# Optimization experiments

Measured on AMD Instinct MI355X. Metric: run time of the kernel, lower is better.

## Reference

```python
import jax, jax.numpy as jnp
import numpy as np

LEAK = 0.01


def setup_inputs() -> dict:
    key = jax.random.key(0)
    k1, k2, k3, k4 = jax.random.split(key, 4)
    N, I, O, H, E = 20000, 128, 128, 4, 320000
    input_h = jax.random.normal(k1, (N, I), dtype=jnp.float32)
    edges = jax.random.randint(k2, (E, 3), 0, N, dtype=jnp.int64)
    # xavier-normal-ish scale for W (H,O,I) and a (H,1,2O)
    W = jax.random.normal(k3, (H, O, I), dtype=jnp.float32) * np.float32(np.sqrt(2.0 / (O + I)))
    a = jax.random.normal(k4, (H, 1, 2 * O), dtype=jnp.float32) * np.float32(np.sqrt(2.0 / (1 + 2 * O)))
    return {"input_h": input_h, "edges": edges, "W": W, "a": a}


def reference(input_h, edges, W, a):
    H, O, _ = W.shape
    N = input_h.shape[0]
    src, rel, dst = edges[:, 0], edges[:, 1], edges[:, 2]
    # per-head projection: x[h,n,o] = sum_i W[h,o,i] * input_h[n,i]
    x = jnp.einsum('hoi,ni->hno', W, input_h)            # (H,N,O)
    h = x.sum(axis=0) / H                                # (N,O)
    # attention scores: (cat([x_src, x_dst]) * a).sum(-1), split a to avoid the concat
    a_src = a[:, 0, :O]                                  # (H,O)
    a_dst = a[:, 0, O:]                                  # (H,O)
    x_dst = x[:, dst]                                    # (H,E,O)
    scores = jnp.einsum('heo,ho->he', x[:, src], a_src) + jnp.einsum('heo,ho->he', x_dst, a_dst)
    # NOTE: faithful to original — softmax is over ALL edges per head
    att = jax.nn.softmax(jax.nn.leaky_relu(scores, LEAK), axis=-1)  # (H,E)
    message = (x_dst * att[..., None]).reshape(-1, O)    # (H*E, O), head-major like torch.cat
    src_rep = jnp.tile(src, H)                           # (H*E,)
    agg = jax.ops.segment_sum(message, src_rep, num_segments=N)  # (N,O)
    return h + agg / H
```

## Files before the change

### kernel.cpp

```cpp
#include <hip/hip_runtime.h>

#define NF 128
#define NH 4
#define BCAP 64

typedef __attribute__((ext_vector_type(4))) float f32x4;
typedef __attribute__((ext_vector_type(8))) short bf16x8;

#define FP4C 0.7f
#define FP4INV (1.0f / FP4C)

__device__ __forceinline__ float b2f(unsigned short u) {
  return __uint_as_float(((unsigned)u) << 16);
}
__device__ __forceinline__ unsigned short f2b(float f) {
  unsigned u = __float_as_uint(f);
  unsigned r = ((u >> 16) & 1u) + 0x7fffu;
  return (unsigned short)((u + r) >> 16);
}

__global__ __launch_bounds__(256) void k_prep0(
    const float* __restrict__ W, unsigned short* __restrict__ Wfhi) {
  int i = blockIdx.x * 256 + threadIdx.x;
  int h = i >> 11, rem = i & 2047;
  int o = rem >> 4, i0 = (rem & 15) * 8;
  const float* p = W + (size_t)(h * NF + o) * NF + i0;
  float4 a = *(const float4*)p, b = *(const float4*)(p + 4);
  float vv[8] = {a.x, a.y, a.z, a.w, b.x, b.y, b.z, b.w};
  bf16x8 hi8;
  #pragma unroll
  for (int j = 0; j < 8; ++j) hi8[j] = (short)f2b(vv[j]);
  int rec = (((o >> 4) * 4 + h) * 4 + (i0 >> 5)) * 64 +
            ((i0 >> 3) & 3) * 16 + (o & 15);
  *(bf16x8*)(Wfhi + (size_t)rec * 8) = hi8;
}

__global__ __launch_bounds__(256) void k1_mfma(
    const float* __restrict__ inp, const unsigned short* __restrict__ Wfhi,
    const float* __restrict__ ag, unsigned int* __restrict__ x4,
    float* __restrict__ s4s, float* __restrict__ s4d,
    float* __restrict__ out, int* __restrict__ cnt, int N) {
  __shared__ unsigned short sAhi[4 * 64 * 8];
  __shared__ unsigned short sAlo[4 * 64 * 8];
  __shared__ unsigned short xL[32 * 64 * 4];
  const int t = threadIdx.x, w = t >> 6, l = t & 63;
  const int col = l & 15, quad = l >> 4;
  const int n0 = blockIdx.x * 16;

  if (t < 16) cnt[n0 + t] = 0;

  {
    const float* p = inp + (size_t)(n0 + col) * NF + w * 32 + quad * 8;
    float4 v0 = *(const float4*)p, v1 = *(const float4*)(p + 4);
    float vv[8] = {v0.x, v0.y, v0.z, v0.w, v1.x, v1.y, v1.z, v1.w};
    bf16x8 hi8, lo8;
    #pragma unroll
    for (int j = 0; j < 8; ++j) {
      unsigned short hi = f2b(vv[j]);
      hi8[j] = (short)hi;
      lo8[j] = (short)f2b(vv[j] - b2f(hi));
    }
    *(bf16x8*)(sAhi + (w * 64 + l) * 8) = hi8;
    *(bf16x8*)(sAlo + (w * 64 + l) * 8) = lo8;
  }
  __syncthreads();

  bf16x8 Ah[4], Al[4];
  #pragma unroll
  for (int s = 0; s < 4; ++s) {
    Ah[s] = *(bf16x8*)(sAhi + (s * 64 + l) * 8);
    Al[s] = *(bf16x8*)(sAlo + (s * 64 + l) * 8);
  }

  float as8[8], ad8[8];
  #pragma unroll
  for (int ot = 0; ot < 8; ++ot) {
    as8[ot] = ag[w * 2 * NF + ot * 16 + col];
    ad8[ot] = ag[w * 2 * NF + NF + ot * 16 + col];
  }

  const bf16x8* WH = (const bf16x8*)Wfhi;
  bf16x8 cur[4];
  #pragma unroll
  for (int s = 0; s < 4; ++s) cur[s] = WH[(size_t)((0 * 4 + w) * 4 + s) * 64 + l];

  float ps[4] = {0.f, 0.f, 0.f, 0.f}, pd[4] = {0.f, 0.f, 0.f, 0.f};
  #pragma unroll
  for (int ot = 0; ot < 8; ++ot) {
    bf16x8 nxt[4];
    if (ot < 7) {
      #pragma unroll
      for (int s = 0; s < 4; ++s)
        nxt[s] = WH[(size_t)(((ot + 1) * 4 + w) * 4 + s) * 64 + l];
    }
    f32x4 acc = {0.f, 0.f, 0.f, 0.f};
    #pragma unroll
    for (int s = 0; s < 4; ++s) {
      acc = __builtin_amdgcn_mfma_f32_16x16x32_bf16(Al[s], cur[s], acc, 0, 0, 0);
      acc = __builtin_amdgcn_mfma_f32_16x16x32_bf16(Ah[s], cur[s], acc, 0, 0, 0);
    }
    ushort4 xs;
    #pragma unroll
    for (int r = 0; r < 4; ++r) {
      ps[r] = fmaf(acc[r], as8[ot], ps[r]);
      pd[r] = fmaf(acc[r], ad8[ot], pd[r]);
    }
    xs.x = f2b(acc[0]); xs.y = f2b(acc[1]);
    xs.z = f2b(acc[2]); xs.w = f2b(acc[3]);
    *(ushort4*)(xL + ((w * 8 + ot) * 64 + l) * 4) = xs;
    if (ot < 7) {
      #pragma unroll
      for (int s = 0; s < 4; ++s) cur[s] = nxt[s];
    }
  }

  #pragma unroll
  for (int m = 1; m < 16; m <<= 1)
    #pragma unroll
    for (int r = 0; r < 4; ++r) {
      ps[r] += __shfl_xor(ps[r], m);
      pd[r] += __shfl_xor(pd[r], m);
    }
  if (col == 0) {
    #pragma unroll
    for (int r = 0; r < 4; ++r) {
      int n = n0 + quad * 4 + r;
      s4s[n * 4 + w] = ps[r];
      s4d[n * 4 + w] = pd[r];
    }
  }
  __syncthreads();

  {
    int c2 = t & 7, qd = (t >> 3) & 3, ot = t >> 5;
    float xv[4][4][2];
    #pragma unroll
    for (int h = 0; h < NH; ++h) {
      int slab = h * 8 + ot;
      ushort4 qa = *(const ushort4*)(xL + (slab * 64 + qd * 16 + c2 * 2) * 4);
      ushort4 qb = *(const ushort4*)(xL + (slab * 64 + qd * 16 + c2 * 2 + 1) * 4);
      xv[h][0][0] = b2f(qa.x); xv[h][1][0] = b2f(qa.y);
      xv[h][2][0] = b2f(qa.z); xv[h][3][0] = b2f(qa.w);
      xv[h][0][1] = b2f(qb.x); xv[h][1][1] = b2f(qb.y);
      xv[h][2][1] = b2f(qb.z); xv[h][3][1] = b2f(qb.w);
    }
    #pragma unroll
    for (int r = 0; r < 4; ++r) {
      int n = n0 + qd * 4 + r;
      float o0 = 0.25f * (xv[0][r][0] + xv[1][r][0] + xv[2][r][0] + xv[3][r][0]);
      float o1 = 0.25f * (xv[0][r][1] + xv[1][r][1] + xv[2][r][1] + xv[3][r][1]);
      *(float2*)(out + (size_t)n * NF + ot * 16 + c2 * 2) = make_float2(o0, o1);
      unsigned q = 0;
      #pragma unroll
      for (int h = 0; h < NH; ++h) {
        int q0 = __float2int_rn(xv[h][r][0] * FP4INV + 7.5f);
        int q1 = __float2int_rn(xv[h][r][1] * FP4INV + 7.5f);
        q0 = q0 < 0 ? 0 : (q0 > 15 ? 15 : q0);
        q1 = q1 < 0 ? 0 : (q1 > 15 ? 15 : q1);
        q |= ((unsigned)q0) << (4 * h);
        q |= ((unsigned)q1) << (4 * (4 + h));
      }
      x4[(size_t)n * 64 + ot * 8 + c2] = q;
    }
  }
}

__global__ __launch_bounds__(256) void k_edge(
    const int* __restrict__ edges, const float4* __restrict__ s4s,
    const float4* __restrict__ s4d, int* __restrict__ cnt,
    uint4* __restrict__ recs, float4* __restrict__ Zpart, int N, int E) {
  __shared__ float4 zsh[4];
  int base = (blockIdx.x * 256 + threadIdx.x) * 2;
  float z0 = 0.f, z1 = 0.f, z2 = 0.f, z3 = 0.f;
  #pragma unroll
  for (int k = 0; k < 2; ++k) {
    int e = base + k;
    if (e < E) {
      int s = edges[3 * (size_t)e];
      int d = edges[3 * (size_t)e + 2];
      float4 ss = s4s[s];
      float4 dd = s4d[d];
      float sc0 = ss.x + dd.x, sc1 = ss.y + dd.y;
      float sc2 = ss.z + dd.z, sc3 = ss.w + dd.w;
      float v0 = __expf(sc0 > 0.f ? sc0 : 0.01f * sc0);
      float v1 = __expf(sc1 > 0.f ? sc1 : 0.01f * sc1);
      float v2 = __expf(sc2 > 0.f ? sc2 : 0.01f * sc2);
      float v3 = __expf(sc3 > 0.f ? sc3 : 0.01f * sc3);
      z0 += v0; z1 += v1; z2 += v2; z3 += v3;
      unsigned evx = (unsigned)f2b(v0) | ((unsigned)f2b(v1) << 16);
      unsigned evy = (unsigned)f2b(v2) | ((unsigned)f2b(v3) << 16);
      int rk = atomicAdd(&cnt[s], 1);
      if (rk < BCAP)
        recs[(size_t)s * BCAP + rk] = make_uint4((unsigned)d, evx, evy, 0u);
    }
  }
  #pragma unroll
  for (int m = 32; m; m >>= 1) {
    z0 += __shfl_xor(z0, m, 64);
    z1 += __shfl_xor(z1, m, 64);
    z2 += __shfl_xor(z2, m, 64);
    z3 += __shfl_xor(z3, m, 64);
  }
  int wv = threadIdx.x >> 6, lane = threadIdx.x & 63;
  if (lane == 0) zsh[wv] = make_float4(z0, z1, z2, z3);
  __syncthreads();
  if (threadIdx.x == 0) {
    float4 a0 = zsh[0], a1 = zsh[1], a2 = zsh[2], a3 = zsh[3];
    Zpart[blockIdx.x] =
        make_float4(a0.x + a1.x + a2.x + a3.x, a0.y + a1.y + a2.y + a3.y,
                    a0.z + a1.z + a2.z + a3.z, a0.w + a1.w + a2.w + a3.w);
  }
}

__global__ __launch_bounds__(256) void k_agg(
    const uint4* __restrict__ recs, const int* __restrict__ cnt,
    const float4* __restrict__ Zpart, int nzp,
    const unsigned int* __restrict__ x4, float* __restrict__ out, int N) {
  __shared__ uint4 rsh[4][BCAP];
  __shared__ float4 zld[4];
  const int t = threadIdx.x, wv = t >> 6, lane = t & 63;

  float z0 = 0.f, z1 = 0.f, z2 = 0.f, z3 = 0.f;
  for (int i = t; i < nzp; i += 256) {
    float4 z = Zpart[i];
    z0 += z.x; z1 += z.y; z2 += z.z; z3 += z.w;
  }
  #pragma unroll
  for (int m = 32; m; m >>= 1) {
    z0 += __shfl_xor(z0, m, 64);
    z1 += __shfl_xor(z1, m, 64);
    z2 += __shfl_xor(z2, m, 64);
    z3 += __shfl_xor(z3, m, 64);
  }
  if (lane == 0) zld[wv] = make_float4(z0, z1, z2, z3);
  __syncthreads();
  {
    float4 a0 = zld[0], a1 = zld[1], a2 = zld[2], a3 = zld[3];
    z0 = 0.25f / (a0.x + a1.x + a2.x + a3.x);
    z1 = 0.25f / (a0.y + a1.y + a2.y + a3.y);
    z2 = 0.25f / (a0.z + a1.z + a2.z + a3.z);
    z3 = 0.25f / (a0.w + a1.w + a2.w + a3.w);
  }

  int n = (int)((blockIdx.x * 256 + t) >> 6);
  if (n >= N) return;
  int deg = cnt[n];
  if (deg == 0) return;
  if (deg > BCAP) deg = BCAP;
  if (lane < deg) rsh[wv][lane] = recs[(size_t)n * BCAP + lane];
  float A00 = 0.f, A01 = 0.f, A10 = 0.f, A11 = 0.f;
  float A20 = 0.f, A21 = 0.f, A30 = 0.f, A31 = 0.f;
  float S0 = 0.f, S1 = 0.f, S2 = 0.f, S3 = 0.f;
  for (int i = 0; i < deg; ++i) {
    uint4 rec = rsh[wv][i];
    unsigned q = x4[(size_t)rec.x * 64 + lane];
    float w0 = b2f((unsigned short)(rec.y & 0xffffu));
    float w1 = b2f((unsigned short)(rec.y >> 16));
    float w2 = b2f((unsigned short)(rec.z & 0xffffu));
    float w3 = b2f((unsigned short)(rec.z >> 16));
    S0 += w0; S1 += w1; S2 += w2; S3 += w3;
    A00 = fmaf(w0, (float)(q & 15u), A00);
    A10 = fmaf(w1, (float)((q >> 4) & 15u), A10);
    A20 = fmaf(w2, (float)((q >> 8) & 15u), A20);
    A30 = fmaf(w3, (float)((q >> 12) & 15u), A30);
    A01 = fmaf(w0, (float)((q >> 16) & 15u), A01);
    A11 = fmaf(w1, (float)((q >> 20) & 15u), A11);
    A21 = fmaf(w2, (float)((q >> 24) & 15u), A21);
    A31 = fmaf(w3, (float)(q >> 28), A31);
  }
  float t0 = z0 * A00 + z1 * A10 + z2 * A20 + z3 * A30;
  float t1 = z0 * A01 + z1 * A11 + z2 * A21 + z3 * A31;
  float sz = z0 * S0 + z1 * S1 + z2 * S2 + z3 * S3;
  float r0 = FP4C * t0 - 7.5f * FP4C * sz;
  float r1 = FP4C * t1 - 7.5f * FP4C * sz;
  float2* op = (float2*)(out + (size_t)n * NF + lane * 2);
  float2 cur = *op;
  cur.x += r0;
  cur.y += r1;
  *op = cur;
}

extern "C" void kernel_launch(void* const* d_in, const int* in_sizes, int n_in,
                              void* d_out, int out_size, void* d_ws, size_t ws_size,
                              hipStream_t stream) {
  const float* inp   = (const float*)d_in[0];
  const int*   edges = (const int*)d_in[1];
  const float* Wg    = (const float*)d_in[2];
  const float* ag    = (const float*)d_in[3];
  float*       out   = (float*)d_out;
  const int N = in_sizes[0] / NF;
  const int E = in_sizes[1] / 3;
  const int nblkE = (E + 511) / 512;

  char* ws = (char*)d_ws;
  size_t off = 0;
  unsigned int* x4 = (unsigned int*)(ws + off); off += (size_t)N * 64 * 4;
  float* s4s = (float*)(ws + off); off += (size_t)N * 4 * 4;
  float* s4d = (float*)(ws + off); off += (size_t)N * 4 * 4;
  uint4* recs = (uint4*)(ws + off); off += (size_t)N * BCAP * 16;
  unsigned short* Wfhi = (unsigned short*)(ws + off); off += (size_t)NH * NF * NF * 2;
  int* cnt = (int*)(ws + off); off += (size_t)N * 4;
  float4* Zpart = (float4*)(ws + off); off += (size_t)nblkE * 16;

  k_prep0<<<32, 256, 0, stream>>>(Wg, Wfhi);
  k1_mfma<<<N / 16, 256, 0, stream>>>(inp, Wfhi, ag, x4, s4s, s4d, out, cnt, N);
  k_edge<<<nblkE, 256, 0, stream>>>(edges, (const float4*)s4s,
                                    (const float4*)s4d, cnt, recs, Zpart, N, E);
  k_agg<<<(N * 64 + 255) / 256, 256, 0, stream>>>(recs, cnt, Zpart, nblkE,
                                                  x4, out, N);
}
```

Before: 136.5 us.

## Accumulate softmax normalizer atomically and unroll edge and aggregation loops by two

The per-block partial softmax sums are replaced by float atomicAdds into four padded global accumulators, zeroed in the prep kernel. Each aggregation block then reads four scalars instead of re-reducing every partial sum with a block barrier. The edge kernel loads edge pairs with vectorized int2 reads and processes two edges explicitly. The aggregation loop is unrolled by two to raise memory-level parallelism on the gathered x4 loads. Float atomics make the normalizer sum order nondeterministic.

Result: faster. 133.2 us (-2.5%).

```diff
diff --git a/kernel.cpp b/kernel.cpp
--- a/kernel.cpp
+++ b/kernel.cpp
@@ -20,7 +20,9 @@
 }
 
 __global__ __launch_bounds__(256) void k_prep0(
-    const float* __restrict__ W, unsigned short* __restrict__ Wfhi) {
+    const float* __restrict__ W, unsigned short* __restrict__ Wfhi,
+    float* __restrict__ Zacc) {
+  if (blockIdx.x == 0 && threadIdx.x < 4) Zacc[threadIdx.x * 32] = 0.f;
   int i = blockIdx.x * 256 + threadIdx.x;
   int h = i >> 11, rem = i & 2047;
   int o = rem >> 4, i0 = (rem & 15) * 8;
@@ -168,31 +170,57 @@
 __global__ __launch_bounds__(256) void k_edge(
     const int* __restrict__ edges, const float4* __restrict__ s4s,
     const float4* __restrict__ s4d, int* __restrict__ cnt,
-    uint4* __restrict__ recs, float4* __restrict__ Zpart, int N, int E) {
+    uint4* __restrict__ recs, float* __restrict__ Zacc, int E) {
   __shared__ float4 zsh[4];
-  int base = (blockIdx.x * 256 + threadIdx.x) * 2;
+  const int g = blockIdx.x * 256 + threadIdx.x;
+  const int base = g * 2;
   float z0 = 0.f, z1 = 0.f, z2 = 0.f, z3 = 0.f;
-  #pragma unroll
-  for (int k = 0; k < 2; ++k) {
-    int e = base + k;
-    if (e < E) {
-      int s = edges[3 * (size_t)e];
-      int d = edges[3 * (size_t)e + 2];
-      float4 ss = s4s[s];
-      float4 dd = s4d[d];
-      float sc0 = ss.x + dd.x, sc1 = ss.y + dd.y;
-      float sc2 = ss.z + dd.z, sc3 = ss.w + dd.w;
-      float v0 = __expf(sc0 > 0.f ? sc0 : 0.01f * sc0);
-      float v1 = __expf(sc1 > 0.f ? sc1 : 0.01f * sc1);
-      float v2 = __expf(sc2 > 0.f ? sc2 : 0.01f * sc2);
-      float v3 = __expf(sc3 > 0.f ? sc3 : 0.01f * sc3);
-      z0 += v0; z1 += v1; z2 += v2; z3 += v3;
-      unsigned evx = (unsigned)f2b(v0) | ((unsigned)f2b(v1) << 16);
-      unsigned evy = (unsigned)f2b(v2) | ((unsigned)f2b(v3) << 16);
-      int rk = atomicAdd(&cnt[s], 1);
-      if (rk < BCAP)
-        recs[(size_t)s * BCAP + rk] = make_uint4((unsigned)d, evx, evy, 0u);
-    }
+  if (base + 1 < E) {
+    const int2* ep = (const int2*)edges + (size_t)g * 3;
+    int2 p0 = ep[0], p1 = ep[1], p2 = ep[2];
+    const int s0 = p0.x, d0 = p1.x, s1 = p1.y, d1 = p2.y;
+    float4 sa = s4s[s0], da = s4d[d0];
+    float4 sb = s4s[s1], db = s4d[d1];
+    float a0 = sa.x + da.x, a1 = sa.y + da.y;
+    float a2 = sa.z + da.z, a3 = sa.w + da.w;
+    float b0 = sb.x + db.x, b1 = sb.y + db.y;
+    float b2v = sb.z + db.z, b3 = sb.w + db.w;
+    float va0 = __expf(a0 > 0.f ? a0 : 0.01f * a0);
+    float va1 = __expf(a1 > 0.f ? a1 : 0.01f * a1);
+    float va2 = __expf(a2 > 0.f ? a2 : 0.01f * a2);
+    float va3 = __expf(a3 > 0.f ? a3 : 0.01f * a3);
+    float vb0 = __expf(b0 > 0.f ? b0 : 0.01f * b0);
+    float vb1 = __expf(b1 > 0.f ? b1 : 0.01f * b1);
+    float vb2 = __expf(b2v > 0.f ? b2v : 0.01f * b2v);
+    float vb3 = __expf(b3 > 0.f ? b3 : 0.01f * b3);
+    z0 = va0 + vb0; z1 = va1 + vb1; z2 = va2 + vb2; z3 = va3 + vb3;
+    unsigned eax = (unsigned)f2b(va0) | ((unsigned)f2b(va1) << 16);
+    unsigned eay = (unsigned)f2b(va2) | ((unsigned)f2b(va3) << 16);
+    unsigned ebx = (unsigned)f2b(vb0) | ((unsigned)f2b(vb1) << 16);
+    unsigned eby = (unsigned)f2b(vb2) | ((unsigned)f2b(vb3) << 16);
+    int ra = atomicAdd(&cnt[s0], 1);
+    if (ra < BCAP)
+      recs[(size_t)s0 * BCAP + ra] = make_uint4((unsigned)d0, eax, eay, 0u);
+    int rb = atomicAdd(&cnt[s1], 1);
+    if (rb < BCAP)
+      recs[(size_t)s1 * BCAP + rb] = make_uint4((unsigned)d1, ebx, eby, 0u);
+  } else if (base < E) {
+    int s = edges[3 * (size_t)base];
+    int d = edges[3 * (size_t)base + 2];
+    float4 ss = s4s[s];
+    float4 dd = s4d[d];
+    float sc0 = ss.x + dd.x, sc1 = ss.y + dd.y;
+    float sc2 = ss.z + dd.z, sc3 = ss.w + dd.w;
+    float v0 = __expf(sc0 > 0.f ? sc0 : 0.01f * sc0);
+    float v1 = __expf(sc1 > 0.f ? sc1 : 0.01f * sc1);
+    float v2 = __expf(sc2 > 0.f ? sc2 : 0.01f * sc2);
+    float v3 = __expf(sc3 > 0.f ? sc3 : 0.01f * sc3);
+    z0 += v0; z1 += v1; z2 += v2; z3 += v3;
+    unsigned evx = (unsigned)f2b(v0) | ((unsigned)f2b(v1) << 16);
+    unsigned evy = (unsigned)f2b(v2) | ((unsigned)f2b(v3) << 16);
+    int rk = atomicAdd(&cnt[s], 1);
+    if (rk < BCAP)
+      recs[(size_t)s * BCAP + rk] = make_uint4((unsigned)d, evx, evy, 0u);
   }
   #pragma unroll
   for (int m = 32; m; m >>= 1) {
@@ -206,52 +234,68 @@
   __syncthreads();
   if (threadIdx.x == 0) {
     float4 a0 = zsh[0], a1 = zsh[1], a2 = zsh[2], a3 = zsh[3];
-    Zpart[blockIdx.x] =
-        make_float4(a0.x + a1.x + a2.x + a3.x, a0.y + a1.y + a2.y + a3.y,
-                    a0.z + a1.z + a2.z + a3.z, a0.w + a1.w + a2.w + a3.w);
+    atomicAdd(&Zacc[0],  a0.x + a1.x + a2.x + a3.x);
+    atomicAdd(&Zacc[32], a0.y + a1.y + a2.y + a3.y);
+    atomicAdd(&Zacc[64], a0.z + a1.z + a2.z + a3.z);
+    atomicAdd(&Zacc[96], a0.w + a1.w + a2.w + a3.w);
   }
 }
 
 __global__ __launch_bounds__(256) void k_agg(
     const uint4* __restrict__ recs, const int* __restrict__ cnt,
-    const float4* __restrict__ Zpart, int nzp,
-    const unsigned int* __restrict__ x4, float* __restrict__ out, int N) {
+    const float* __restrict__ Zacc, const unsigned int* __restrict__ x4,
+    float* __restrict__ out, int N) {
   __shared__ uint4 rsh[4][BCAP];
-  __shared__ float4 zld[4];
   const int t = threadIdx.x, wv = t >> 6, lane = t & 63;
-
-  float z0 = 0.f, z1 = 0.f, z2 = 0.f, z3 = 0.f;
-  for (int i = t; i < nzp; i += 256) {
-    float4 z = Zpart[i];
-    z0 += z.x; z1 += z.y; z2 += z.z; z3 += z.w;
-  }
-  #pragma unroll
-  for (int m = 32; m; m >>= 1) {
-    z0 += __shfl_xor(z0, m, 64);
-    z1 += __shfl_xor(z1, m, 64);
-    z2 += __shfl_xor(z2, m, 64);
-    z3 += __shfl_xor(z3, m, 64);
-  }
-  if (lane == 0) zld[wv] = make_float4(z0, z1, z2, z3);
-  __syncthreads();
-  {
-    float4 a0 = zld[0], a1 = zld[1], a2 = zld[2], a3 = zld[3];
-    z0 = 0.25f / (a0.x + a1.x + a2.x + a3.x);
-    z1 = 0.25f / (a0.y + a1.y + a2.y + a3.y);
-    z2 = 0.25f / (a0.z + a1.z + a2.z + a3.z);
-    z3 = 0.25f / (a0.w + a1.w + a2.w + a3.w);
-  }
 
   int n = (int)((blockIdx.x * 256 + t) >> 6);
   if (n >= N) return;
   int deg = cnt[n];
   if (deg == 0) return;
   if (deg > BCAP) deg = BCAP;
+
+  const float z0 = 0.25f / Zacc[0];
+  const float z1 = 0.25f / Zacc[32];
+  const float z2 = 0.25f / Zacc[64];
+  const float z3 = 0.25f / Zacc[96];
+
   if (lane < deg) rsh[wv][lane] = recs[(size_t)n * BCAP + lane];
   float A00 = 0.f, A01 = 0.f, A10 = 0.f, A11 = 0.f;
   float A20 = 0.f, A21 = 0.f, A30 = 0.f, A31 = 0.f;
   float S0 = 0.f, S1 = 0.f, S2 = 0.f, S3 = 0.f;
-  for (int i = 0; i < deg; ++i) {
+  int i = 0;
+  for (; i + 1 < deg; i += 2) {
+    uint4 ra = rsh[wv][i];
+    uint4 rb = rsh[wv][i + 1];
+    unsigned qa = x4[(size_t)ra.x * 64 + lane];
+    unsigned qb = x4[(size_t)rb.x * 64 + lane];
+    float w0a = b2f((unsigned short)(ra.y & 0xffffu));
+    float w1a = b2f((unsigned short)(ra.y >> 16));
+    float w2a = b2f((unsigned short)(ra.z & 0xffffu));
+    float w3a = b2f((unsigned short)(ra.z >> 16));
+    float w0b = b2f((unsigned short)(rb.y & 0xffffu));
+    float w1b = b2f((unsigned short)(rb.y >> 16));
+    float w2b = b2f((unsigned short)(rb.z & 0xffffu));
+    float w3b = b2f((unsigned short)(rb.z >> 16));
+    S0 += w0a + w0b; S1 += w1a + w1b; S2 += w2a + w2b; S3 += w3a + w3b;
+    A00 = fmaf(w0a, (float)(qa & 15u), A00);
+    A10 = fmaf(w1a, (float)((qa >> 4) & 15u), A10);
+    A20 = fmaf(w2a, (float)((qa >> 8) & 15u), A20);
+    A30 = fmaf(w3a, (float)((qa >> 12) & 15u), A30);
+    A01 = fmaf(w0a, (float)((qa >> 16) & 15u), A01);
+    A11 = fmaf(w1a, (float)((qa >> 20) & 15u), A11);
+    A21 = fmaf(w2a, (float)((qa >> 24) & 15u), A21);
+    A31 = fmaf(w3a, (float)(qa >> 28), A31);
+    A00 = fmaf(w0b, (float)(qb & 15u), A00);
+    A10 = fmaf(w1b, (float)((qb >> 4) & 15u), A10);
+    A20 = fmaf(w2b, (float)((qb >> 8) & 15u), A20);
+    A30 = fmaf(w3b, (float)((qb >> 12) & 15u), A30);
+    A01 = fmaf(w0b, (float)((qb >> 16) & 15u), A01);
+    A11 = fmaf(w1b, (float)((qb >> 20) & 15u), A11);
+    A21 = fmaf(w2b, (float)((qb >> 24) & 15u), A21);
+    A31 = fmaf(w3b, (float)(qb >> 28), A31);
+  }
+  if (i < deg) {
     uint4 rec = rsh[wv][i];
     unsigned q = x4[(size_t)rec.x * 64 + lane];
     float w0 = b2f((unsigned short)(rec.y & 0xffffu));
@@ -300,12 +344,11 @@
   uint4* recs = (uint4*)(ws + off); off += (size_t)N * BCAP * 16;
   unsigned short* Wfhi = (unsigned short*)(ws + off); off += (size_t)NH * NF * NF * 2;
   int* cnt = (int*)(ws + off); off += (size_t)N * 4;
-  float4* Zpart = (float4*)(ws + off); off += (size_t)nblkE * 16;
-
-  k_prep0<<<32, 256, 0, stream>>>(Wg, Wfhi);
+  float* Zacc = (float*)(ws + off); off += 128 * 4;
+
+  k_prep0<<<32, 256, 0, stream>>>(Wg, Wfhi, Zacc);
   k1_mfma<<<N / 16, 256, 0, stream>>>(inp, Wfhi, ag, x4, s4s, s4d, out, cnt, N);
   k_edge<<<nblkE, 256, 0, stream>>>(edges, (const float4*)s4s,
-                                    (const float4*)s4d, cnt, recs, Zpart, N, E);
-  k_agg<<<(N * 64 + 255) / 256, 256, 0, stream>>>(recs, cnt, Zpart, nblkE,
-                                                  x4, out, N);
-}
+                                    (const float4*)s4d, cnt, recs, Zacc, E);
+  k_agg<<<(N * 64 + 255) / 256, 256, 0, stream>>>(recs, cnt, Zacc, x4, out, N);
+}
```
